# Kernel tuning notes

Hardware: AMD Instinct MI355X
Metric: run time of the kernel (lower is better)

## Reference

```python
import jax, jax.numpy as jnp
import numpy as np

N = 100000
E = 1600000
IN_DIM, HID, NCLS = 256, 128, 40


def setup_inputs() -> dict:
    key = jax.random.key(0)
    ks = jax.random.split(key, 8)
    x = jax.random.normal(ks[0], (N, IN_DIM), dtype=jnp.float32)
    edge_index = jax.random.randint(ks[1], (2, E), 0, N, dtype=jnp.int32)
    def glorot(k, shape):
        lim = float(np.sqrt(6.0 / (shape[0] + shape[1])))
        return jax.random.uniform(k, shape, jnp.float32, -lim, lim)
    return {
        "x": x,
        "edge_index": edge_index,
        "W1": glorot(ks[2], (IN_DIM, HID)), "b1": jnp.zeros((HID,), jnp.float32),
        "W2": glorot(ks[3], (HID, HID)),    "b2": jnp.zeros((HID,), jnp.float32),
        "W3": glorot(ks[4], (HID, NCLS)),   "b3": jnp.zeros((NCLS,), jnp.float32),
    }


def _gcn_conv(x, src, dst, W, b):
    # dense transform first (PyG GCNConv applies lin before propagate)
    h = x @ W  # [N, out]
    # symmetric normalization with self-loops: deg over destination (in-degree)
    ones = jnp.ones(src.shape[0], dtype=x.dtype)
    deg = jax.ops.segment_sum(ones, dst, num_segments=N)
    dinv = jnp.where(deg > 0, jax.lax.rsqrt(jnp.maximum(deg, 1e-12)), 0.0)
    norm = dinv[src] * dinv[dst]  # [E+N]
    msgs = h[src] * norm[:, None]  # gather + scale
    out = jax.ops.segment_sum(msgs, dst, num_segments=N)
    return out + b


def reference(x, edge_index, W1, b1, W2, b2, W3, b3):
    # add self-loops once (same for every layer)
    loop = jnp.arange(N, dtype=edge_index.dtype)
    src = jnp.concatenate([edge_index[0], loop])
    dst = jnp.concatenate([edge_index[1], loop])
    h = _gcn_conv(x, src, dst, W1, b1)
    h = jax.nn.relu(h)  # dropout is identity in eval mode
    h = _gcn_conv(h, src, dst, W2, b2)
    h = jax.nn.relu(h)
    h = _gcn_conv(h, src, dst, W3, b3)
    return h
```

## Files before the change

### kernel.cpp

```cpp
#include <hip/hip_runtime.h>
#include <hip/hip_bf16.h>


#define WAVE 64
#define SLOTS 48
#define FILL_NR 8
#define FILL_NCHUNK 784

typedef short short8v __attribute__((ext_vector_type(8)));
typedef float f32x4 __attribute__((ext_vector_type(4)));

__device__ inline void split_bf16(float v, ushort& hi, ushort& lo) {
    __hip_bfloat16 h = __float2bfloat16(v);
    float hf = __bfloat162float(h);
    __hip_bfloat16 l = __float2bfloat16(v - hf);
    hi = *reinterpret_cast<ushort*>(&h);
    lo = *reinterpret_cast<ushort*>(&l);
}

__device__ inline float bf2f(ushort u) {
    unsigned int t = ((unsigned int)u) << 16;
    return __uint_as_float(t);
}

__device__ inline ushort f2bf(float v) {
    __hip_bfloat16 h = __float2bfloat16(v);
    return *reinterpret_cast<ushort*>(&h);
}


__global__ void k_fill_part(const int* __restrict__ src, const int* __restrict__ dst,
                            int* __restrict__ cnt, int* __restrict__ slots,
                            int E, int N) {
    int b = blockIdx.x;
    int r = b & (FILL_NR - 1);
    int c = b >> 3;
    int lo = (int)((long long)E * c / FILL_NCHUNK);
    int hi = (int)((long long)E * (c + 1) / FILL_NCHUNK);
    int rlo = (int)((long long)N * r / FILL_NR);
    int rhi = (int)((long long)N * (r + 1) / FILL_NR);
    for (int e = lo + threadIdx.x; e < hi; e += 256) {
        int d = dst[e];
        if (d >= rlo && d < rhi) {
            int p = atomicAdd(&cnt[d], 1);
            if (p < SLOTS) slots[(size_t)d * SLOTS + p] = src[e];
        }
    }
}

__global__ void k_dinv(const int* __restrict__ cnt, float* __restrict__ dinv, int N) {
    int i = blockIdx.x * blockDim.x + threadIdx.x;
    if (i < N) dinv[i] = rsqrtf((float)cnt[i] + 1.0f);
}


__global__ void k_wsplit(const float* __restrict__ W, ushort* __restrict__ Wth,
                         ushort* __restrict__ Wtl, int K, int M, int Mpad) {
    int idx = blockIdx.x * 256 + threadIdx.x;
    if (idx >= K * Mpad) return;
    int k = idx / Mpad, m = idx % Mpad;
    float v = (m < M) ? W[(size_t)k * M + m] : 0.f;
    ushort h, l;
    split_bf16(v, h, l);
    Wth[(size_t)m * K + k] = h;
    Wtl[(size_t)m * K + k] = l;
}


template <int K, bool BF16OUT>
__global__ __launch_bounds__(256) void gemm_mfma128(const float* __restrict__ A,
                                                    const ushort* __restrict__ Wth,
                                                    const ushort* __restrict__ Wtl,
                                                    const float* __restrict__ rowscale,
                                                    void* __restrict__ outv, int N) {
    constexpr int KC = 32;
    constexpr int LD = 40;
    __shared__ ushort Ah[128 * LD], Al[128 * LD], Bh[128 * LD], Bl[128 * LD];

    const int tid = threadIdx.x;
    const int lane = tid & 63, wave = tid >> 6;
    const int wr = (wave & 1) * 64, wc = (wave >> 1) * 64;
    const int r0 = blockIdx.x * 128;
    const int tr = lane & 15, quad = lane >> 4;

    f32x4 acc[4][4];
#pragma unroll
    for (int i = 0; i < 4; ++i)
#pragma unroll
        for (int j = 0; j < 4; ++j) acc[i][j] = (f32x4)(0.f);

    for (int kc = 0; kc < K; kc += KC) {
        for (int f = tid; f < 128 * 8; f += 256) {
            int row = f >> 3, kq = f & 7;
            int grow = r0 + row;
            if (grow > N - 1) grow = N - 1;
            float4 v = *reinterpret_cast<const float4*>(A + (size_t)grow * K + kc + kq * 4);
            ushort h0, l0, h1, l1, h2, l2, h3, l3;
            split_bf16(v.x, h0, l0);
            split_bf16(v.y, h1, l1);
            split_bf16(v.z, h2, l2);
            split_bf16(v.w, h3, l3);
            *reinterpret_cast<ushort4*>(&Ah[row * LD + kq * 4]) = make_ushort4(h0, h1, h2, h3);
            *reinterpret_cast<ushort4*>(&Al[row * LD + kq * 4]) = make_ushort4(l0, l1, l2, l3);
        }
        for (int f = tid; f < 512; f += 256) {
            int col = f >> 2, part = f & 3;
            *reinterpret_cast<uint4*>(&Bh[col * LD + part * 8]) =
                *reinterpret_cast<const uint4*>(Wth + (size_t)col * K + kc + part * 8);
            *reinterpret_cast<uint4*>(&Bl[col * LD + part * 8]) =
                *reinterpret_cast<const uint4*>(Wtl + (size_t)col * K + kc + part * 8);
        }
        __syncthreads();
        short8v ah[4], al[4], bh[4], bl[4];
#pragma unroll
        for (int i = 0; i < 4; ++i) {
            ah[i] = *reinterpret_cast<const short8v*>(&Ah[(wr + i * 16 + tr) * LD + quad * 8]);
            al[i] = *reinterpret_cast<const short8v*>(&Al[(wr + i * 16 + tr) * LD + quad * 8]);
            bh[i] = *reinterpret_cast<const short8v*>(&Bh[(wc + i * 16 + tr) * LD + quad * 8]);
            bl[i] = *reinterpret_cast<const short8v*>(&Bl[(wc + i * 16 + tr) * LD + quad * 8]);
        }
#pragma unroll
        for (int i = 0; i < 4; ++i)
#pragma unroll
            for (int j = 0; j < 4; ++j) {
                acc[i][j] = __builtin_amdgcn_mfma_f32_16x16x32_bf16(ah[i], bh[j], acc[i][j], 0, 0, 0);
                acc[i][j] = __builtin_amdgcn_mfma_f32_16x16x32_bf16(ah[i], bl[j], acc[i][j], 0, 0, 0);
                acc[i][j] = __builtin_amdgcn_mfma_f32_16x16x32_bf16(al[i], bh[j], acc[i][j], 0, 0, 0);
            }
        __syncthreads();
    }

#pragma unroll
    for (int i = 0; i < 4; ++i) {
        int rbase = r0 + wr + i * 16 + quad * 4;
        float rs[4];
#pragma unroll
        for (int reg = 0; reg < 4; ++reg) {
            int r = rbase + reg;
            rs[reg] = (r < N) ? rowscale[r] : 0.f;
        }
#pragma unroll
        for (int j = 0; j < 4; ++j) {
            int c = wc + j * 16 + tr;
#pragma unroll
            for (int reg = 0; reg < 4; ++reg) {
                int r = rbase + reg;
                if (r < N) {
                    float v = acc[i][j][reg] * rs[reg];
                    if (BF16OUT)
                        ((ushort*)outv)[(size_t)r * 128 + c] = f2bf(v);
                    else
                        ((float*)outv)[(size_t)r * 128 + c] = v;
                }
            }
        }
    }
}


__global__ __launch_bounds__(256) void gemm_mfma40(const float* __restrict__ A,
                                                   const ushort* __restrict__ Wth,
                                                   const ushort* __restrict__ Wtl,
                                                   const float* __restrict__ rowscale,
                                                   float* __restrict__ out, int N) {
    constexpr int K = 128, KC = 32, LD = 40, M = 40;
    __shared__ ushort Ah[128 * LD], Al[128 * LD], Bh[48 * LD], Bl[48 * LD];

    const int tid = threadIdx.x;
    const int lane = tid & 63, wave = tid >> 6;
    const int wr = wave * 32;
    const int r0 = blockIdx.x * 128;
    const int tr = lane & 15, quad = lane >> 4;

    f32x4 acc[2][3];
#pragma unroll
    for (int i = 0; i < 2; ++i)
#pragma unroll
        for (int j = 0; j < 3; ++j) acc[i][j] = (f32x4)(0.f);

    for (int kc = 0; kc < K; kc += KC) {
        for (int f = tid; f < 128 * 8; f += 256) {
            int row = f >> 3, kq = f & 7;
            int grow = r0 + row;
            if (grow > N - 1) grow = N - 1;
            float4 v = *reinterpret_cast<const float4*>(A + (size_t)grow * K + kc + kq * 4);
            ushort h0, l0, h1, l1, h2, l2, h3, l3;
            split_bf16(v.x, h0, l0);
            split_bf16(v.y, h1, l1);
            split_bf16(v.z, h2, l2);
            split_bf16(v.w, h3, l3);
            *reinterpret_cast<ushort4*>(&Ah[row * LD + kq * 4]) = make_ushort4(h0, h1, h2, h3);
            *reinterpret_cast<ushort4*>(&Al[row * LD + kq * 4]) = make_ushort4(l0, l1, l2, l3);
        }
        for (int f = tid; f < 192; f += 256) {
            int col = f >> 2, part = f & 3;
            *reinterpret_cast<uint4*>(&Bh[col * LD + part * 8]) =
                *reinterpret_cast<const uint4*>(Wth + (size_t)col * K + kc + part * 8);
            *reinterpret_cast<uint4*>(&Bl[col * LD + part * 8]) =
                *reinterpret_cast<const uint4*>(Wtl + (size_t)col * K + kc + part * 8);
        }
        __syncthreads();
        short8v ah[2], al[2], bh[3], bl[3];
#pragma unroll
        for (int i = 0; i < 2; ++i) {
            ah[i] = *reinterpret_cast<const short8v*>(&Ah[(wr + i * 16 + tr) * LD + quad * 8]);
            al[i] = *reinterpret_cast<const short8v*>(&Al[(wr + i * 16 + tr) * LD + quad * 8]);
        }
#pragma unroll
        for (int j = 0; j < 3; ++j) {
            bh[j] = *reinterpret_cast<const short8v*>(&Bh[(j * 16 + tr) * LD + quad * 8]);
            bl[j] = *reinterpret_cast<const short8v*>(&Bl[(j * 16 + tr) * LD + quad * 8]);
        }
#pragma unroll
        for (int i = 0; i < 2; ++i)
#pragma unroll
            for (int j = 0; j < 3; ++j) {
                acc[i][j] = __builtin_amdgcn_mfma_f32_16x16x32_bf16(ah[i], bh[j], acc[i][j], 0, 0, 0);
                acc[i][j] = __builtin_amdgcn_mfma_f32_16x16x32_bf16(ah[i], bl[j], acc[i][j], 0, 0, 0);
                acc[i][j] = __builtin_amdgcn_mfma_f32_16x16x32_bf16(al[i], bh[j], acc[i][j], 0, 0, 0);
            }
        __syncthreads();
    }

#pragma unroll
    for (int i = 0; i < 2; ++i) {
        int rbase = r0 + wr + i * 16 + quad * 4;
        float rs[4];
#pragma unroll
        for (int reg = 0; reg < 4; ++reg) {
            int r = rbase + reg;
            rs[reg] = (r < N) ? rowscale[r] : 0.f;
        }
#pragma unroll
        for (int j = 0; j < 3; ++j) {
            int c = j * 16 + tr;
#pragma unroll
            for (int reg = 0; reg < 4; ++reg) {
                int r = rbase + reg;
                if (r < N && c < M) out[(size_t)r * M + c] = acc[i][j][reg] * rs[reg];
            }
        }
    }
}


template <bool RELU>
__global__ __launch_bounds__(256) void agg128_bf2(const ushort* __restrict__ S,
                                                  const int* __restrict__ slots,
                                                  const int* __restrict__ cnt,
                                                  const float* __restrict__ dinv,
                                                  const float* __restrict__ bias,
                                                  float* __restrict__ out, int N) {
    int w = (blockIdx.x * blockDim.x + threadIdx.x) >> 6;
    int lane = threadIdx.x & 63;
    int npair = (N + 1) >> 1;
    if (w >= npair) return;
    int half = lane >> 5, sub = lane & 31;
    int node = 2 * w + half;
    bool valid = node < N;
    int snode = valid ? node : 0;
    const ushort4* S4 = (const ushort4*)S;
    const int* row = slots + (size_t)snode * SLOTS;
    int c = valid ? cnt[snode] : 0;
    if (c > SLOTS) c = SLOTS;
    int cmax = max(c, __shfl(c, lane ^ 32));

    ushort4 sv = S4[(size_t)snode * 32 + sub];
    float a0 = bf2f(sv.x), a1 = bf2f(sv.y), a2 = bf2f(sv.z), a3 = bf2f(sv.w);

    int e = 0;
    for (; e + 8 <= cmax; e += 8) {
        int s[8];
#pragma unroll
        for (int u = 0; u < 8; ++u) s[u] = (e + u < c) ? row[e + u] : snode;
        ushort4 v[8];
#pragma unroll
        for (int u = 0; u < 8; ++u) v[u] = S4[(size_t)s[u] * 32 + sub];
#pragma unroll
        for (int u = 0; u < 8; ++u) {
            float m = (e + u < c) ? 1.f : 0.f;
            a0 += m * bf2f(v[u].x);
            a1 += m * bf2f(v[u].y);
            a2 += m * bf2f(v[u].z);
            a3 += m * bf2f(v[u].w);
        }
    }
    for (; e < cmax; ++e) {
        int s = (e < c) ? row[e] : snode;
        ushort4 v = S4[(size_t)s * 32 + sub];
        float m = (e < c) ? 1.f : 0.f;
        a0 += m * bf2f(v.x);
        a1 += m * bf2f(v.y);
        a2 += m * bf2f(v.z);
        a3 += m * bf2f(v.w);
    }

    if (valid) {
        float di = dinv[node];
        float4 bv = ((const float4*)bias)[sub];
        float o0 = a0 * di + bv.x;
        float o1 = a1 * di + bv.y;
        float o2 = a2 * di + bv.z;
        float o3 = a3 * di + bv.w;
        if (RELU) {
            o0 = fmaxf(o0, 0.f);
            o1 = fmaxf(o1, 0.f);
            o2 = fmaxf(o2, 0.f);
            o3 = fmaxf(o3, 0.f);
        }
        ((float4*)out)[(size_t)node * 32 + sub] = make_float4(o0, o1, o2, o3);
    }
}

__global__ __launch_bounds__(256) void agg40(const float* __restrict__ S,
                                             const int* __restrict__ slots,
                                             const int* __restrict__ cnt,
                                             const float* __restrict__ dinv,
                                             const float* __restrict__ bias,
                                             float* __restrict__ out, int N) {
    int wid = (blockIdx.x * blockDim.x + threadIdx.x) >> 6;
    int lane = threadIdx.x & 63;
    if (wid >= N || lane >= 40) return;
    const int* row = slots + (size_t)wid * SLOTS;
    int c = cnt[wid];
    if (c > SLOTS) c = SLOTS;
    float acc = S[(size_t)wid * 40 + lane];
    int e = 0;
    for (; e + 8 <= c; e += 8) {
        int s[8];
#pragma unroll
        for (int u = 0; u < 8; ++u) s[u] = row[e + u];
        float v[8];
#pragma unroll
        for (int u = 0; u < 8; ++u) v[u] = S[(size_t)s[u] * 40 + lane];
#pragma unroll
        for (int u = 0; u < 8; ++u) acc += v[u];
    }
    for (; e < c; ++e) acc += S[(size_t)row[e] * 40 + lane];
    out[(size_t)wid * 40 + lane] = acc * dinv[wid] + bias[lane];
}


extern "C" void kernel_launch(void* const* d_in, const int* in_sizes, int n_in,
                              void* d_out, int out_size, void* d_ws, size_t ws_size,
                              hipStream_t stream) {
    const float* x  = (const float*)d_in[0];
    const int*   ei = (const int*)d_in[1];
    const float* W1 = (const float*)d_in[2];
    const float* b1 = (const float*)d_in[3];
    const float* W2 = (const float*)d_in[4];
    const float* b2 = (const float*)d_in[5];
    const float* W3 = (const float*)d_in[6];
    const float* b3 = (const float*)d_in[7];
    float* out = (float*)d_out;

    const int IN_DIM = 256, HID = 128;
    const int N = in_sizes[0] / IN_DIM;
    const int E = in_sizes[1] / 2;
    const int* srcE = ei;
    const int* dstE = ei + E;

    char* ws = (char*)d_ws;
    size_t off = 0;
    auto alloc = [&](size_t bytes) -> void* {
        off = (off + 255) & ~(size_t)255;
        void* p = ws + off;
        off += bytes;
        return p;
    };
    int*    cnt   = (int*)alloc((size_t)N * 4);
    float*  dinv  = (float*)alloc((size_t)N * 4);
    int*    slots = (int*)alloc((size_t)N * SLOTS * 4);
    ushort* bufS  = (ushort*)alloc((size_t)N * HID * 4);
    float*  bufH  = (float*)alloc((size_t)N * HID * 4);
    ushort* W1th  = (ushort*)alloc((size_t)128 * 256 * 2);
    ushort* W1tl  = (ushort*)alloc((size_t)128 * 256 * 2);
    ushort* W2th  = (ushort*)alloc((size_t)128 * 128 * 2);
    ushort* W2tl  = (ushort*)alloc((size_t)128 * 128 * 2);
    ushort* W3th  = (ushort*)alloc((size_t)48 * 128 * 2);
    ushort* W3tl  = (ushort*)alloc((size_t)48 * 128 * 2);

    const int NB = (N + 255) / 256;
    const int AGGB = (N * WAVE + 255) / 256;
    const int AGG2B = (((N + 1) / 2) * WAVE + 255) / 256;
    const int GB = (N + 127) / 128;
    const int FB = FILL_NR * FILL_NCHUNK;

    k_wsplit<<<(256 * 128 + 255) / 256, 256, 0, stream>>>(W1, W1th, W1tl, 256, 128, 128);
    k_wsplit<<<(128 * 128 + 255) / 256, 256, 0, stream>>>(W2, W2th, W2tl, 128, 128, 128);
    k_wsplit<<<(128 * 48 + 255) / 256, 256, 0, stream>>>(W3, W3th, W3tl, 128, 40, 48);

    hipMemsetAsync(cnt, 0, (size_t)N * 4, stream);
    k_fill_part<<<FB, 256, 0, stream>>>(srcE, dstE, cnt, slots, E, N);
    k_dinv<<<NB, 256, 0, stream>>>(cnt, dinv, N);

    gemm_mfma128<256, true><<<GB, 256, 0, stream>>>(x, W1th, W1tl, dinv, bufS, N);
    agg128_bf2<true><<<AGG2B, 256, 0, stream>>>(bufS, slots, cnt, dinv, b1, bufH, N);
    gemm_mfma128<128, true><<<GB, 256, 0, stream>>>(bufH, W2th, W2tl, dinv, bufS, N);
    agg128_bf2<true><<<AGG2B, 256, 0, stream>>>(bufS, slots, cnt, dinv, b2, bufH, N);
    gemm_mfma40<<<GB, 256, 0, stream>>>(bufH, W3th, W3tl, dinv, (float*)bufS, N);
    agg40<<<AGGB, 256, 0, stream>>>((float*)bufS, slots, cnt, dinv, b3, out, N);
}
```

Baseline: 590.1 us.

## Prefetch next GEMM K-chunk into registers and widen aggregation to 4 nodes per wave

Both MFMA GEMM kernels now load the next K-chunk of A and the split weights into registers right after the barrier. This overlaps global-memory latency with the MFMA work on the current chunk, at the cost of extra registers. The 128-wide bf16 aggregation kernel now handles four nodes per wave, with 16 lanes per node each reading 16-byte uint4 (8 bf16) instead of 8-byte loads. This gives wider gather loads and more rows in flight. The loop bound becomes the max degree across the four nodes, so lanes with fewer neighbours may do more masked work.

```diff
diff --git a/kernel.cpp b/kernel.cpp
--- a/kernel.cpp
+++ b/kernel.cpp
@@ -22,6 +22,9 @@
     unsigned int t = ((unsigned int)u) << 16;
     return __uint_as_float(t);
 }
+
+__device__ inline float bfLo(unsigned int u) { return __uint_as_float(u << 16); }
+__device__ inline float bfHi(unsigned int u) { return __uint_as_float(u & 0xffff0000u); }
 
 __device__ inline ushort f2bf(float v) {
     __hip_bfloat16 h = __float2bfloat16(v);
@@ -89,12 +92,33 @@
 #pragma unroll
         for (int j = 0; j < 4; ++j) acc[i][j] = (f32x4)(0.f);
 
-    for (int kc = 0; kc < K; kc += KC) {
-        for (int f = tid; f < 128 * 8; f += 256) {
+    float4 pa[4];
+    uint4 pbh[2], pbl[2];
+    auto loadc = [&](int kc) {
+#pragma unroll
+        for (int u = 0; u < 4; ++u) {
+            int f = tid + u * 256;
             int row = f >> 3, kq = f & 7;
             int grow = r0 + row;
             if (grow > N - 1) grow = N - 1;
-            float4 v = *reinterpret_cast<const float4*>(A + (size_t)grow * K + kc + kq * 4);
+            pa[u] = *reinterpret_cast<const float4*>(A + (size_t)grow * K + kc + kq * 4);
+        }
+#pragma unroll
+        for (int u = 0; u < 2; ++u) {
+            int f = tid + u * 256;
+            int col = f >> 2, part = f & 3;
+            pbh[u] = *reinterpret_cast<const uint4*>(Wth + (size_t)col * K + kc + part * 8);
+            pbl[u] = *reinterpret_cast<const uint4*>(Wtl + (size_t)col * K + kc + part * 8);
+        }
+    };
+
+    loadc(0);
+    for (int kc = 0; kc < K; kc += KC) {
+#pragma unroll
+        for (int u = 0; u < 4; ++u) {
+            int f = tid + u * 256;
+            int row = f >> 3, kq = f & 7;
+            float4 v = pa[u];
             ushort h0, l0, h1, l1, h2, l2, h3, l3;
             split_bf16(v.x, h0, l0);
             split_bf16(v.y, h1, l1);
@@ -103,14 +127,15 @@
             *reinterpret_cast<ushort4*>(&Ah[row * LD + kq * 4]) = make_ushort4(h0, h1, h2, h3);
             *reinterpret_cast<ushort4*>(&Al[row * LD + kq * 4]) = make_ushort4(l0, l1, l2, l3);
         }
-        for (int f = tid; f < 512; f += 256) {
+#pragma unroll
+        for (int u = 0; u < 2; ++u) {
+            int f = tid + u * 256;
             int col = f >> 2, part = f & 3;
-            *reinterpret_cast<uint4*>(&Bh[col * LD + part * 8]) =
-                *reinterpret_cast<const uint4*>(Wth + (size_t)col * K + kc + part * 8);
-            *reinterpret_cast<uint4*>(&Bl[col * LD + part * 8]) =
-                *reinterpret_cast<const uint4*>(Wtl + (size_t)col * K + kc + part * 8);
+            *reinterpret_cast<uint4*>(&Bh[col * LD + part * 8]) = pbh[u];
+            *reinterpret_cast<uint4*>(&Bl[col * LD + part * 8]) = pbl[u];
         }
         __syncthreads();
+        if (kc + KC < K) loadc(kc + KC);
         short8v ah[4], al[4], bh[4], bl[4];
 #pragma unroll
         for (int i = 0; i < 4; ++i) {
@@ -171,6 +196,7 @@
     const int wr = wave * 32;
     const int r0 = blockIdx.x * 128;
     const int tr = lane & 15, quad = lane >> 4;
+    const bool hasb = tid < 192;
 
     f32x4 acc[2][3];
 #pragma unroll
@@ -178,12 +204,31 @@
 #pragma unroll
         for (int j = 0; j < 3; ++j) acc[i][j] = (f32x4)(0.f);
 
-    for (int kc = 0; kc < K; kc += KC) {
-        for (int f = tid; f < 128 * 8; f += 256) {
+    float4 pa[4];
+    uint4 pbh0, pbl0;
+    auto loadc = [&](int kc) {
+#pragma unroll
+        for (int u = 0; u < 4; ++u) {
+            int f = tid + u * 256;
             int row = f >> 3, kq = f & 7;
             int grow = r0 + row;
             if (grow > N - 1) grow = N - 1;
-            float4 v = *reinterpret_cast<const float4*>(A + (size_t)grow * K + kc + kq * 4);
+            pa[u] = *reinterpret_cast<const float4*>(A + (size_t)grow * K + kc + kq * 4);
+        }
+        if (hasb) {
+            int col = tid >> 2, part = tid & 3;
+            pbh0 = *reinterpret_cast<const uint4*>(Wth + (size_t)col * K + kc + part * 8);
+            pbl0 = *reinterpret_cast<const uint4*>(Wtl + (size_t)col * K + kc + part * 8);
+        }
+    };
+
+    loadc(0);
+    for (int kc = 0; kc < K; kc += KC) {
+#pragma unroll
+        for (int u = 0; u < 4; ++u) {
+            int f = tid + u * 256;
+            int row = f >> 3, kq = f & 7;
+            float4 v = pa[u];
             ushort h0, l0, h1, l1, h2, l2, h3, l3;
             split_bf16(v.x, h0, l0);
             split_bf16(v.y, h1, l1);
@@ -192,14 +237,13 @@
             *reinterpret_cast<ushort4*>(&Ah[row * LD + kq * 4]) = make_ushort4(h0, h1, h2, h3);
             *reinterpret_cast<ushort4*>(&Al[row * LD + kq * 4]) = make_ushort4(l0, l1, l2, l3);
         }
-        for (int f = tid; f < 192; f += 256) {
-            int col = f >> 2, part = f & 3;
-            *reinterpret_cast<uint4*>(&Bh[col * LD + part * 8]) =
-                *reinterpret_cast<const uint4*>(Wth + (size_t)col * K + kc + part * 8);
-            *reinterpret_cast<uint4*>(&Bl[col * LD + part * 8]) =
-                *reinterpret_cast<const uint4*>(Wtl + (size_t)col * K + kc + part * 8);
+        if (hasb) {
+            int col = tid >> 2, part = tid & 3;
+            *reinterpret_cast<uint4*>(&Bh[col * LD + part * 8]) = pbh0;
+            *reinterpret_cast<uint4*>(&Bl[col * LD + part * 8]) = pbl0;
         }
         __syncthreads();
+        if (kc + KC < K) loadc(kc + KC);
         short8v ah[2], al[2], bh[3], bl[3];
 #pragma unroll
         for (int i = 0; i < 2; ++i) {
@@ -245,7 +289,7 @@
 
 
 template <bool RELU>
-__global__ __launch_bounds__(256) void agg128_bf2(const ushort* __restrict__ S,
+__global__ __launch_bounds__(256) void agg128_bf4(const ushort* __restrict__ S,
                                                   const int* __restrict__ slots,
                                                   const int* __restrict__ cnt,
                                                   const float* __restrict__ dinv,
@@ -253,62 +297,70 @@
                                                   float* __restrict__ out, int N) {
     int w = (blockIdx.x * blockDim.x + threadIdx.x) >> 6;
     int lane = threadIdx.x & 63;
-    int npair = (N + 1) >> 1;
-    if (w >= npair) return;
-    int half = lane >> 5, sub = lane & 31;
-    int node = 2 * w + half;
+    int nquad = (N + 3) >> 2;
+    if (w >= nquad) return;
+    int part = lane >> 4, sub = lane & 15;
+    int node = 4 * w + part;
     bool valid = node < N;
     int snode = valid ? node : 0;
-    const ushort4* S4 = (const ushort4*)S;
+    const uint4* S8 = (const uint4*)S;
     const int* row = slots + (size_t)snode * SLOTS;
     int c = valid ? cnt[snode] : 0;
     if (c > SLOTS) c = SLOTS;
-    int cmax = max(c, __shfl(c, lane ^ 32));
-
-    ushort4 sv = S4[(size_t)snode * 32 + sub];
-    float a0 = bf2f(sv.x), a1 = bf2f(sv.y), a2 = bf2f(sv.z), a3 = bf2f(sv.w);
+    int cm = max(c, __shfl(c, lane ^ 16));
+    cm = max(cm, __shfl(cm, lane ^ 32));
+
+    uint4 sv = S8[(size_t)snode * 16 + sub];
+    float a0 = bfLo(sv.x), a1 = bfHi(sv.x), a2 = bfLo(sv.y), a3 = bfHi(sv.y);
+    float a4 = bfLo(sv.z), a5 = bfHi(sv.z), a6 = bfLo(sv.w), a7 = bfHi(sv.w);
 
     int e = 0;
-    for (; e + 8 <= cmax; e += 8) {
+    for (; e + 8 <= cm; e += 8) {
         int s[8];
 #pragma unroll
         for (int u = 0; u < 8; ++u) s[u] = (e + u < c) ? row[e + u] : snode;
-        ushort4 v[8];
-#pragma unroll
-        for (int u = 0; u < 8; ++u) v[u] = S4[(size_t)s[u] * 32 + sub];
+        uint4 v[8];
+#pragma unroll
+        for (int u = 0; u < 8; ++u) v[u] = S8[(size_t)s[u] * 16 + sub];
 #pragma unroll
         for (int u = 0; u < 8; ++u) {
             float m = (e + u < c) ? 1.f : 0.f;
-            a0 += m * bf2f(v[u].x);
-            a1 += m * bf2f(v[u].y);
-            a2 += m * bf2f(v[u].z);
-            a3 += m * bf2f(v[u].w);
-        }
-    }
-    for (; e < cmax; ++e) {
+            a0 += m * bfLo(v[u].x);
+            a1 += m * bfHi(v[u].x);
+            a2 += m * bfLo(v[u].y);
+            a3 += m * bfHi(v[u].y);
+            a4 += m * bfLo(v[u].z);
+            a5 += m * bfHi(v[u].z);
+            a6 += m * bfLo(v[u].w);
+            a7 += m * bfHi(v[u].w);
+        }
+    }
+    for (; e < cm; ++e) {
         int s = (e < c) ? row[e] : snode;
-        ushort4 v = S4[(size_t)s * 32 + sub];
+        uint4 v = S8[(size_t)s * 16 + sub];
         float m = (e < c) ? 1.f : 0.f;
-        a0 += m * bf2f(v.x);
-        a1 += m * bf2f(v.y);
-        a2 += m * bf2f(v.z);
-        a3 += m * bf2f(v.w);
+        a0 += m * bfLo(v.x);
+        a1 += m * bfHi(v.x);
+        a2 += m * bfLo(v.y);
+        a3 += m * bfHi(v.y);
+        a4 += m * bfLo(v.z);
+        a5 += m * bfHi(v.z);
+        a6 += m * bfLo(v.w);
+        a7 += m * bfHi(v.w);
     }
 
     if (valid) {
         float di = dinv[node];
-        float4 bv = ((const float4*)bias)[sub];
-        float o0 = a0 * di + bv.x;
-        float o1 = a1 * di + bv.y;
-        float o2 = a2 * di + bv.z;
-        float o3 = a3 * di + bv.w;
+        float4 b0 = ((const float4*)bias)[sub * 2];
+        float4 b1 = ((const float4*)bias)[sub * 2 + 1];
+        float o0 = a0 * di + b0.x, o1 = a1 * di + b0.y, o2 = a2 * di + b0.z, o3 = a3 * di + b0.w;
+        float o4 = a4 * di + b1.x, o5 = a5 * di + b1.y, o6 = a6 * di + b1.z, o7 = a7 * di + b1.w;
         if (RELU) {
-            o0 = fmaxf(o0, 0.f);
-            o1 = fmaxf(o1, 0.f);
-            o2 = fmaxf(o2, 0.f);
-            o3 = fmaxf(o3, 0.f);
-        }
-        ((float4*)out)[(size_t)node * 32 + sub] = make_float4(o0, o1, o2, o3);
+            o0 = fmaxf(o0, 0.f); o1 = fmaxf(o1, 0.f); o2 = fmaxf(o2, 0.f); o3 = fmaxf(o3, 0.f);
+            o4 = fmaxf(o4, 0.f); o5 = fmaxf(o5, 0.f); o6 = fmaxf(o6, 0.f); o7 = fmaxf(o7, 0.f);
+        }
+        ((float4*)out)[(size_t)node * 32 + sub * 2] = make_float4(o0, o1, o2, o3);
+        ((float4*)out)[(size_t)node * 32 + sub * 2 + 1] = make_float4(o4, o5, o6, o7);
     }
 }
 
@@ -382,7 +434,7 @@
 
     const int NB = (N + 255) / 256;
     const int AGGB = (N * WAVE + 255) / 256;
-    const int AGG2B = (((N + 1) / 2) * WAVE + 255) / 256;
+    const int AGG4B = (((N + 3) / 4) * WAVE + 255) / 256;
     const int GB = (N + 127) / 128;
     const int FB = FILL_NR * FILL_NCHUNK;
 
@@ -395,9 +447,9 @@
     k_dinv<<<NB, 256, 0, stream>>>(cnt, dinv, N);
 
     gemm_mfma128<256, true><<<GB, 256, 0, stream>>>(x, W1th, W1tl, dinv, bufS, N);
-    agg128_bf2<true><<<AGG2B, 256, 0, stream>>>(bufS, slots, cnt, dinv, b1, bufH, N);
+    agg128_bf4<true><<<AGG4B, 256, 0, stream>>>(bufS, slots, cnt, dinv, b1, bufH, N);
     gemm_mfma128<128, true><<<GB, 256, 0, stream>>>(bufH, W2th, W2tl, dinv, bufS, N);
-    agg128_bf2<true><<<AGG2B, 256, 0, stream>>>(bufS, slots, cnt, dinv, b2, bufH, N);
+    agg128_bf4<true><<<AGG4B, 256, 0, stream>>>(bufS, slots, cnt, dinv, b2, bufH, N);
     gemm_mfma40<<<GB, 256, 0, stream>>>(bufH, W3th, W3tl, dinv, (float*)bufS, N);
     agg40<<<AGGB, 256, 0, stream>>>((float*)bufS, slots, cnt, dinv, b3, out, N);
 }
```

Result: no change. 592.1 us (+0.3%).
